# Kernel tuning notes

Measured on AMD Instinct MI355X. Metric: run time of the kernel, lower is better.

Reference implementation:

```python
import jax, jax.numpy as jnp
import numpy as np

B, S, HID, NH = 4, 1024, 1024, 16
HD = HID // NH  # 64


def setup_inputs() -> dict:
    key = jax.random.key(0)
    ks = jax.random.split(key, 8)
    scale = 0.02
    return {
        "attention_mask": jnp.zeros((B, 1, 1, S), dtype=jnp.float32),
        "query": jax.random.normal(ks[0], (B, S, HID), dtype=jnp.float32),
        "key": jax.random.normal(ks[1], (B, S, HID), dtype=jnp.float32),
        "value": jax.random.normal(ks[2], (B, S, HID), dtype=jnp.float32),
        "Wq": jax.random.normal(ks[3], (HID, HID), dtype=jnp.float32) * scale,
        "bq": jnp.zeros((HID,), dtype=jnp.float32),
        "Wk": jax.random.normal(ks[4], (HID, HID), dtype=jnp.float32) * scale,
        "bk": jnp.zeros((HID,), dtype=jnp.float32),
    }


def reference(attention_mask, query, key, value, Wq, bq, Wk, bk):
    # Linear projections (torch Linear: x @ W.T + b)
    q = query @ Wq.T + bq  # [B,S,HID]
    k = key @ Wk.T + bk    # [B,S,HID]
    # split heads -> [B,NH,S,HD]
    q = q.reshape(B, S, NH, HD).transpose(0, 2, 1, 3)
    k = k.reshape(B, S, NH, HD).transpose(0, 2, 1, 3)
    scores = jnp.einsum("bhqd,bhkd->bhqk", q, k) / jnp.sqrt(jnp.float32(HD))
    scores = scores + attention_mask  # additive mask broadcast [B,1,1,S]
    probs = jax.nn.softmax(scores, axis=-1)  # [B,NH,S,S]
    # V is shared across heads; head-mean folds into a single contraction:
    # mean_h(probs_h @ V) = (sum_h probs_h) @ V / NH
    out = jnp.einsum("bhqk,bkv->bqv", probs, value) / NH  # [B,S,HID]
    return out
```

## Files before the change

kernel.cpp:

```cpp
#include <hip/hip_runtime.h>
#include <hip/hip_fp16.h>

#define B_    4
#define S_    1024
#define HID_  1024
#define NH_   16
#define HD_   64

#define LOG2E 1.44269504f
#define PSTR  40

typedef _Float16 half8 __attribute__((ext_vector_type(8)));
typedef float f32x4 __attribute__((ext_vector_type(4)));

__device__ __forceinline__ half8 cvt8(float4 a, float4 b) {
    half8 h;
    h[0] = (_Float16)a.x; h[1] = (_Float16)a.y;
    h[2] = (_Float16)a.z; h[3] = (_Float16)a.w;
    h[4] = (_Float16)b.x; h[5] = (_Float16)b.y;
    h[6] = (_Float16)b.z; h[7] = (_Float16)b.w;
    return h;
}

__device__ __forceinline__ float fexp2(float x) {
#if __has_builtin(__builtin_amdgcn_exp2f)
    return __builtin_amdgcn_exp2f(x);
#else
    float r;
    asm("v_exp_f32 %0, %1\n\ts_nop 0" : "=v"(r) : "v"(x));
    return r;
#endif
}

__device__ __forceinline__ void lds_barrier() {
    asm volatile("s_waitcnt lgkmcnt(0)" ::: "memory");
    __builtin_amdgcn_s_barrier();
    __builtin_amdgcn_sched_barrier(0);
}

__device__ __forceinline__ void gll16(const _Float16* g, _Float16* l) {
    __builtin_amdgcn_global_load_lds(
        (const __attribute__((address_space(1))) unsigned int*)g,
        (__attribute__((address_space(3))) unsigned int*)l, 16, 0, 0);
}

__global__ __launch_bounds__(256) void cast_f16(
    const float* __restrict__ query, const float* __restrict__ key,
    const float* __restrict__ Wq, const float* __restrict__ Wk,
    _Float16* __restrict__ Af16, _Float16* __restrict__ Wf16)
{
    const int x = blockIdx.x;
    if (blockIdx.y == 0) {
        long base = ((long)x * 256 + threadIdx.x) * 8;
        const float* src = (x < 2048) ? (query + base) : (key + base - (4l << 20));
        float4 v0 = *(const float4*)src, v1 = *(const float4*)(src + 4);
        *(half8*)(Af16 + base) = cvt8(v0, v1);
    } else {
        if (x >= 1024) return;
        long base = ((long)x * 256 + threadIdx.x) * 8;
        const float* src = (x < 512) ? (Wq + base) : (Wk + base - (1l << 20));
        float4 v0 = *(const float4*)src, v1 = *(const float4*)(src + 4);
        *(half8*)(Wf16 + base) = cvt8(v0, v1);
    }
}

__global__ __launch_bounds__(256) void proj_qk_f16(
    const _Float16* __restrict__ Af16,
    const _Float16* __restrict__ Wf16,
    const float* __restrict__ bq, const float* __restrict__ bk,
    _Float16* __restrict__ Oq, _Float16* __restrict__ Ok)
{
    const int f  = blockIdx.x + 16 * blockIdx.y + 512 * blockIdx.z;
    const int w2 = (f & 7) * 128 + (f >> 3);
    const int bx = w2 & 15, by = (w2 >> 4) & 31, bz = w2 >> 9;

    const _Float16* A    = Af16 + (long)bz * 4096 * 1024;
    const _Float16* Wm   = Wf16 + (long)bz * 1024 * 1024;
    const float*    bias = bz ? bk : bq;
    _Float16*       Co   = bz ? Ok : Oq;

    __shared__ _Float16 Al[2][128 * 32];
    __shared__ _Float16 Bl[2][64 * 32];

    const int tid  = threadIdx.x;
    const int wv   = tid >> 6;
    const int lane = tid & 63;
    const int l15  = lane & 15;
    const int quad = lane >> 4;
    const int wm   = wv & 1, wn = wv >> 1;
    const int m0   = by * 128, n0 = bx * 64;

    const int srA  = (lane >> 2);
    const int scA  = (lane & 3) * 8;
    const _Float16* gA0 = A  + (long)(m0 + wv * 16 + srA) * 1024 + scA;
    const _Float16* gA1 = A  + (long)(m0 + 64 + wv * 16 + srA) * 1024 + scA;
    const _Float16* gB  = Wm + (long)(n0 + wv * 16 + srA) * 1024 + scA;
    const int ldsW = wv * 512;

    f32x4 acc[4][2];
#pragma unroll
    for (int i = 0; i < 4; i++)
#pragma unroll
        for (int j = 0; j < 2; j++) acc[i][j] = (f32x4){0.f, 0.f, 0.f, 0.f};

    gll16(gA0, &Al[0][ldsW]);
    gll16(gA1, &Al[0][2048 + ldsW]);
    gll16(gB,  &Bl[0][ldsW]);
    __syncthreads();

#pragma unroll 2
    for (int kt = 0; kt < HID_; kt += 32) {
        const int p = (kt >> 5) & 1;

        if (kt + 32 < HID_) {
            gll16(gA0 + kt + 32, &Al[p ^ 1][ldsW]);
            gll16(gA1 + kt + 32, &Al[p ^ 1][2048 + ldsW]);
            gll16(gB  + kt + 32, &Bl[p ^ 1][ldsW]);
        }

        half8 af[4], bf[2];
#pragma unroll
        for (int i = 0; i < 4; i++)
            af[i] = *(const half8*)(&Al[p][(wm * 64 + i * 16 + l15) * 32 + quad * 8]);
#pragma unroll
        for (int j = 0; j < 2; j++)
            bf[j] = *(const half8*)(&Bl[p][(wn * 32 + j * 16 + l15) * 32 + quad * 8]);

#pragma unroll
        for (int i = 0; i < 4; i++)
#pragma unroll
            for (int j = 0; j < 2; j++)
                acc[i][j] = __builtin_amdgcn_mfma_f32_16x16x32_f16(
                    af[i], bf[j], acc[i][j], 0, 0, 0);

        __syncthreads();
    }

    const int isQ = (bz == 0);
#pragma unroll
    for (int j = 0; j < 2; j++) {
        int col = n0 + wn * 32 + j * 16 + l15;
        float bv = bias[col];
        int h = col >> 6, d = col & 63, pp = d >> 3, jj = d & 7;
#pragma unroll
        for (int i = 0; i < 4; i++) {
            int row = m0 + wm * 64 + i * 16 + quad * 4;
            int bb = row >> 10, ss = row & 1023;
            long base;
            if (isQ)
                base = ((((long)(bb * NH_ + h) * 64 + (ss >> 4)) * 8 + pp) * 16
                        + (ss & 15)) * 8 + jj;
            else
                base = (((long)(bb * NH_ + h) * 8 + pp) * 1024 + ss) * 8 + jj;
#pragma unroll
            for (int r = 0; r < 4; r++)
                Co[base + r * 8] = (_Float16)(acc[i][j][r] + bv);
        }
    }
}

__global__ __launch_bounds__(512) void attn_psum_f16(
    const _Float16* __restrict__ qb,
    const _Float16* __restrict__ kb,
    const float* __restrict__ mask,
    _Float16* __restrict__ P)
{
    const int f   = blockIdx.x + 64 * blockIdx.y + 256 * blockIdx.z;
    const int w2s = (f & 7) * 128 + (f >> 3);
    const int qt  = w2s & 63;
    const int b   = (w2s >> 6) & 3;
    const int hz  = w2s >> 8;

    const int q0   = qt * 16;
    const int tid  = threadIdx.x;
    const int w    = tid >> 6;
    const int lane = tid & 63;
    const int l15  = lane & 15;
    const int quad = lane >> 4;

    __shared__ float redS[2][16][8];

    const float SC = 0.125f * LOG2E;

    float mreg[8];
#pragma unroll
    for (int t = 0; t < 8; t++)
        mreg[t] = mask[b * S_ + t * 128 + w * 16 + l15] * LOG2E;

    f32x4 acc[8];
#pragma unroll
    for (int t = 0; t < 8; t++) acc[t] = (f32x4){0.f, 0.f, 0.f, 0.f};

    for (int ii = 0; ii < 4; ii++) {
        const int h = hz * 4 + ii;
        const _Float16* qh = qb + ((long)(b * NH_ + h) * 64 + qt) * 1024;
        const _Float16* kh = kb + (long)(b * NH_ + h) * 8192 * 8;

        half8 a0 = *(const half8*)(qh + quad * 128 + l15 * 8);
        half8 a1 = *(const half8*)(qh + (quad + 4) * 128 + l15 * 8);

        f32x4 s[8];
#pragma unroll
        for (int cc = 0; cc < 8; cc++) {
            const int key = cc * 128 + w * 16 + l15;
            half8 b0 = *(const half8*)(kh + (long)quad * 8192 + key * 8);
            half8 b1 = *(const half8*)(kh + (long)(quad + 4) * 8192 + key * 8);
            f32x4 c = (f32x4){0.f, 0.f, 0.f, 0.f};
            c = __builtin_amdgcn_mfma_f32_16x16x32_f16(a0, b0, c, 0, 0, 0);
            c = __builtin_amdgcn_mfma_f32_16x16x32_f16(a1, b1, c, 0, 0, 0);
            s[cc] = c;
        }

        const int p = ii & 1;
        float sm[4] = {0.f, 0.f, 0.f, 0.f};
#pragma unroll
        for (int t = 0; t < 8; t++)
#pragma unroll
            for (int r = 0; r < 4; r++) {
                float pr = fexp2(fmaf(s[t][r], SC, mreg[t]));
                s[t][r] = pr;
                sm[r] += pr;
            }
#pragma unroll
        for (int off = 1; off < 16; off <<= 1)
#pragma unroll
            for (int r = 0; r < 4; r++) sm[r] += __shfl_xor(sm[r], off);
        if (l15 == 0)
#pragma unroll
            for (int r = 0; r < 4; r++) redS[p][quad * 4 + r][w] = sm[r];
        __syncthreads();

#pragma unroll
        for (int r = 0; r < 4; r++) {
            float4 v0 = *(float4*)&redS[p][quad * 4 + r][0];
            float4 v1 = *(float4*)&redS[p][quad * 4 + r][4];
            float tot = (v0.x + v0.y + v0.z + v0.w) + (v1.x + v1.y + v1.z + v1.w);
            float inv = 1.f / tot;
#pragma unroll
            for (int t = 0; t < 8; t++) acc[t][r] += s[t][r] * inv;
        }
    }

    _Float16* prow = P + (long)hz * ((long)B_ * S_ * S_) + (long)(b * S_ + q0) * S_;
#pragma unroll
    for (int t = 0; t < 8; t++)
#pragma unroll
        for (int r = 0; r < 4; r++) {
            int row = quad * 4 + r;
            prow[(long)row * S_ + t * 128 + w * 16 + l15] = (_Float16)acc[t][r];
        }
}

__global__ __launch_bounds__(256) void vt_combine(
    const _Float16* __restrict__ P, _Float16* __restrict__ o,
    const float* __restrict__ V, _Float16* __restrict__ Vt)
{
    __shared__ float t[32][33];
    if (blockIdx.y == 0) {
        if (blockIdx.x >= 2048) return;
        const long QS = (long)B_ * S_ * S_;
        long i = (long)(blockIdx.x * 256 + threadIdx.x) * 8;
        half8 a = *(const half8*)(P + i);
        half8 b = *(const half8*)(P + QS + i);
        half8 c = *(const half8*)(P + 2 * QS + i);
        half8 d = *(const half8*)(P + 3 * QS + i);
        half8 r;
#pragma unroll
        for (int e = 0; e < 8; e++)
            r[e] = (_Float16)((float)a[e] + (float)b[e] + (float)c[e] + (float)d[e]);
        *(half8*)(o + i) = r;
    } else {
        const int x  = blockIdx.x;
        const int b  = x >> 10;
        const int s0 = ((x >> 5) & 31) * 32;
        const int h0 = (x & 31) * 32;
        const int tx = threadIdx.x & 31, ty = threadIdx.x >> 5;
#pragma unroll
        for (int rr = 0; rr < 4; rr++) {
            int s = s0 + ty + rr * 8;
            t[ty + rr * 8][tx] = V[((long)b * S_ + s) * HID_ + h0 + tx];
        }
        __syncthreads();
#pragma unroll
        for (int rr = 0; rr < 4; rr++) {
            int h = h0 + ty + rr * 8;
            Vt[((long)b * HID_ + h) * S_ + s0 + tx] = (_Float16)t[tx][ty + rr * 8];
        }
    }
}

__global__ __launch_bounds__(256) void pv_f16(
    const _Float16* __restrict__ Pc,
    const _Float16* __restrict__ Vt,
    float* __restrict__ out)
{
    const int f   = blockIdx.x + 16 * blockIdx.y + 128 * blockIdx.z;
    const int xcd = f & 7, ii = f >> 3;
    const int bx  = ii & 15;
    const int by  = (ii >> 4) + ((xcd & 1) << 2);
    const int b   = xcd >> 1;

    const _Float16* A  = Pc + (long)b * S_ * S_;
    const _Float16* Bm = Vt + (long)b * HID_ * S_;

    __shared__ _Float16 Al[2][128 * PSTR];
    __shared__ _Float16 Bl[2][64 * PSTR];

    const int tid  = threadIdx.x;
    const int wv   = tid >> 6;
    const int lane = tid & 63;
    const int l15  = lane & 15;
    const int quad = lane >> 4;
    const int wm   = wv & 1, wn = wv >> 1;
    const int m0   = by * 128, n0 = bx * 64;
    const int sr   = tid >> 2;
    const int sc   = (tid & 3) * 8;

    const _Float16* ap0 = A  + (long)(m0 + sr) * S_ + sc;
    const _Float16* ap1 = A  + (long)(m0 + 64 + sr) * S_ + sc;
    const _Float16* bp0 = Bm + (long)(n0 + sr) * S_ + sc;

    f32x4 acc[4][2];
#pragma unroll
    for (int i = 0; i < 4; i++)
#pragma unroll
        for (int j = 0; j < 2; j++) acc[i][j] = (f32x4){0.f, 0.f, 0.f, 0.f};

    half8 ca0 = *(const half8*)(ap0);
    half8 ca1 = *(const half8*)(ap1);
    half8 cb0 = *(const half8*)(bp0);
    *(half8*)&Al[0][sr * PSTR + sc] = ca0;
    *(half8*)&Al[0][(64 + sr) * PSTR + sc] = ca1;
    *(half8*)&Bl[0][sr * PSTR + sc] = cb0;
    ca0 = *(const half8*)(ap0 + 32);
    ca1 = *(const half8*)(ap1 + 32);
    cb0 = *(const half8*)(bp0 + 32);
    lds_barrier();

#pragma unroll 2
    for (int kt = 0; kt < S_; kt += 32) {
        const int p = (kt >> 5) & 1;

        half8 na0 = ca0, na1 = ca1, nb0 = cb0;
        if (kt + 64 < S_) {
            na0 = *(const half8*)(ap0 + kt + 64);
            na1 = *(const half8*)(ap1 + kt + 64);
            nb0 = *(const half8*)(bp0 + kt + 64);
        }

        half8 af[4], bfm[2];
#pragma unroll
        for (int i = 0; i < 4; i++)
            af[i] = *(const half8*)(&Al[p][(wm * 64 + i * 16 + l15) * PSTR + quad * 8]);
#pragma unroll
        for (int j = 0; j < 2; j++)
            bfm[j] = *(const half8*)(&Bl[p][(wn * 32 + j * 16 + l15) * PSTR + quad * 8]);

        if (kt + 32 < S_) {
            *(half8*)&Al[p ^ 1][sr * PSTR + sc] = ca0;
            *(half8*)&Al[p ^ 1][(64 + sr) * PSTR + sc] = ca1;
            *(half8*)&Bl[p ^ 1][sr * PSTR + sc] = cb0;
        }

#pragma unroll
        for (int i = 0; i < 4; i++)
#pragma unroll
            for (int j = 0; j < 2; j++)
                acc[i][j] = __builtin_amdgcn_mfma_f32_16x16x32_f16(
                    af[i], bfm[j], acc[i][j], 0, 0, 0);

        lds_barrier();
        ca0 = na0; ca1 = na1; cb0 = nb0;
    }

    const float alpha = 1.f / NH_;
#pragma unroll
    for (int i = 0; i < 4; i++) {
        int row = m0 + wm * 64 + i * 16 + quad * 4;
#pragma unroll
        for (int j = 0; j < 2; j++) {
            int col = n0 + wn * 32 + j * 16 + l15;
#pragma unroll
            for (int r = 0; r < 4; r++)
                out[(long)(b * S_ + row + r) * HID_ + col] = acc[i][j][r] * alpha;
        }
    }
}

extern "C" void kernel_launch(void* const* d_in, const int* in_sizes, int n_in,
                              void* d_out, int out_size, void* d_ws, size_t ws_size,
                              hipStream_t stream)
{
    const float* mask  = (const float*)d_in[0];
    const float* query = (const float*)d_in[1];
    const float* key   = (const float*)d_in[2];
    const float* value = (const float*)d_in[3];
    const float* Wq    = (const float*)d_in[4];
    const float* bq    = (const float*)d_in[5];
    const float* Wk    = (const float*)d_in[6];
    const float* bk    = (const float*)d_in[7];
    float* out = (float*)d_out;

    char* ws = (char*)d_ws;
    const long MB = 1l << 20;
    _Float16* qbuf = (_Float16*)(ws);
    _Float16* kbuf = (_Float16*)(ws + 8 * MB);
    _Float16* Af16 = (_Float16*)(ws + 16 * MB);
    _Float16* Wf16 = (_Float16*)(ws + 32 * MB);
    _Float16* Pq   = (_Float16*)(ws + 16 * MB);
    _Float16* Vt   = (_Float16*)(ws);
    _Float16* psum = (_Float16*)(ws + 8 * MB);

    cast_f16<<<dim3(4096, 2), dim3(256), 0, stream>>>(
        query, key, Wq, Wk, Af16, Wf16);

    proj_qk_f16<<<dim3(16, 32, 2), dim3(256), 0, stream>>>(
        Af16, Wf16, bq, bk, qbuf, kbuf);

    attn_psum_f16<<<dim3(S_ / 16, B_, 4), dim3(512), 0, stream>>>(
        qbuf, kbuf, mask, Pq);

    vt_combine<<<dim3(4096, 2), dim3(256), 0, stream>>>(Pq, psum, value, Vt);

    pv_f16<<<dim3(HID_ / 64, S_ / 128, B_), dim3(256), 0, stream>>>(psum, Vt, out);
}
```

Before: 196.3 us.

## Sum all heads in one attention pass, move V transpose into cast, use direct-to-LDS loads

The attention kernel now loops over all 16 heads per block and writes the head-summed probabilities directly. This removes the four partial P buffers and the separate combine pass, along with their large memory traffic. The V transpose moves into the cast kernel, and the PV GEMM switches to global_load_lds direct-to-LDS loads with an unpadded layout. The cost is a much smaller attention grid (256 blocks of 512 threads), which may underfill the GPU and serialize 16 heads per block. The unpadded LDS layout may also cause bank conflicts.

```diff
diff --git a/kernel.cpp b/kernel.cpp
--- a/kernel.cpp
+++ b/kernel.cpp
@@ -8,7 +8,6 @@
 #define HD_   64
 
 #define LOG2E 1.44269504f
-#define PSTR  40
 
 typedef _Float16 half8 __attribute__((ext_vector_type(8)));
 typedef float f32x4 __attribute__((ext_vector_type(4)));
@@ -32,12 +31,6 @@
 #endif
 }
 
-__device__ __forceinline__ void lds_barrier() {
-    asm volatile("s_waitcnt lgkmcnt(0)" ::: "memory");
-    __builtin_amdgcn_s_barrier();
-    __builtin_amdgcn_sched_barrier(0);
-}
-
 __device__ __forceinline__ void gll16(const _Float16* g, _Float16* l) {
     __builtin_amdgcn_global_load_lds(
         (const __attribute__((address_space(1))) unsigned int*)g,
@@ -47,20 +40,39 @@
 __global__ __launch_bounds__(256) void cast_f16(
     const float* __restrict__ query, const float* __restrict__ key,
     const float* __restrict__ Wq, const float* __restrict__ Wk,
-    _Float16* __restrict__ Af16, _Float16* __restrict__ Wf16)
-{
+    const float* __restrict__ V,
+    _Float16* __restrict__ Af16, _Float16* __restrict__ Wf16,
+    _Float16* __restrict__ Vt)
+{
+    __shared__ float t[32][33];
     const int x = blockIdx.x;
     if (blockIdx.y == 0) {
         long base = ((long)x * 256 + threadIdx.x) * 8;
         const float* src = (x < 2048) ? (query + base) : (key + base - (4l << 20));
         float4 v0 = *(const float4*)src, v1 = *(const float4*)(src + 4);
         *(half8*)(Af16 + base) = cvt8(v0, v1);
-    } else {
+    } else if (blockIdx.y == 1) {
         if (x >= 1024) return;
         long base = ((long)x * 256 + threadIdx.x) * 8;
         const float* src = (x < 512) ? (Wq + base) : (Wk + base - (1l << 20));
         float4 v0 = *(const float4*)src, v1 = *(const float4*)(src + 4);
         *(half8*)(Wf16 + base) = cvt8(v0, v1);
+    } else {
+        const int b  = x >> 10;
+        const int s0 = ((x >> 5) & 31) * 32;
+        const int h0 = (x & 31) * 32;
+        const int tx = threadIdx.x & 31, ty = threadIdx.x >> 5;
+#pragma unroll
+        for (int rr = 0; rr < 4; rr++) {
+            int s = s0 + ty + rr * 8;
+            t[ty + rr * 8][tx] = V[((long)b * S_ + s) * HID_ + h0 + tx];
+        }
+        __syncthreads();
+#pragma unroll
+        for (int rr = 0; rr < 4; rr++) {
+            int h = h0 + ty + rr * 8;
+            Vt[((long)b * HID_ + h) * S_ + s0 + tx] = (_Float16)t[tx][ty + rr * 8];
+        }
     }
 }
 
@@ -163,13 +175,12 @@
     const _Float16* __restrict__ qb,
     const _Float16* __restrict__ kb,
     const float* __restrict__ mask,
-    _Float16* __restrict__ P)
-{
-    const int f   = blockIdx.x + 64 * blockIdx.y + 256 * blockIdx.z;
-    const int w2s = (f & 7) * 128 + (f >> 3);
+    _Float16* __restrict__ psum)
+{
+    const int f   = blockIdx.x + 64 * blockIdx.y;
+    const int w2s = (f & 7) * 32 + (f >> 3);
     const int qt  = w2s & 63;
-    const int b   = (w2s >> 6) & 3;
-    const int hz  = w2s >> 8;
+    const int b   = w2s >> 6;
 
     const int q0   = qt * 16;
     const int tid  = threadIdx.x;
@@ -191,8 +202,7 @@
 #pragma unroll
     for (int t = 0; t < 8; t++) acc[t] = (f32x4){0.f, 0.f, 0.f, 0.f};
 
-    for (int ii = 0; ii < 4; ii++) {
-        const int h = hz * 4 + ii;
+    for (int h = 0; h < NH_; h++) {
         const _Float16* qh = qb + ((long)(b * NH_ + h) * 64 + qt) * 1024;
         const _Float16* kh = kb + (long)(b * NH_ + h) * 8192 * 8;
 
@@ -211,7 +221,7 @@
             s[cc] = c;
         }
 
-        const int p = ii & 1;
+        const int p = h & 1;
         float sm[4] = {0.f, 0.f, 0.f, 0.f};
 #pragma unroll
         for (int t = 0; t < 8; t++)
@@ -241,7 +251,7 @@
         }
     }
 
-    _Float16* prow = P + (long)hz * ((long)B_ * S_ * S_) + (long)(b * S_ + q0) * S_;
+    _Float16* prow = psum + (long)(b * S_ + q0) * S_;
 #pragma unroll
     for (int t = 0; t < 8; t++)
 #pragma unroll
@@ -249,44 +259,6 @@
             int row = quad * 4 + r;
             prow[(long)row * S_ + t * 128 + w * 16 + l15] = (_Float16)acc[t][r];
         }
-}
-
-__global__ __launch_bounds__(256) void vt_combine(
-    const _Float16* __restrict__ P, _Float16* __restrict__ o,
-    const float* __restrict__ V, _Float16* __restrict__ Vt)
-{
-    __shared__ float t[32][33];
-    if (blockIdx.y == 0) {
-        if (blockIdx.x >= 2048) return;
-        const long QS = (long)B_ * S_ * S_;
-        long i = (long)(blockIdx.x * 256 + threadIdx.x) * 8;
-        half8 a = *(const half8*)(P + i);
-        half8 b = *(const half8*)(P + QS + i);
-        half8 c = *(const half8*)(P + 2 * QS + i);
-        half8 d = *(const half8*)(P + 3 * QS + i);
-        half8 r;
-#pragma unroll
-        for (int e = 0; e < 8; e++)
-            r[e] = (_Float16)((float)a[e] + (float)b[e] + (float)c[e] + (float)d[e]);
-        *(half8*)(o + i) = r;
-    } else {
-        const int x  = blockIdx.x;
-        const int b  = x >> 10;
-        const int s0 = ((x >> 5) & 31) * 32;
-        const int h0 = (x & 31) * 32;
-        const int tx = threadIdx.x & 31, ty = threadIdx.x >> 5;
-#pragma unroll
-        for (int rr = 0; rr < 4; rr++) {
-            int s = s0 + ty + rr * 8;
-            t[ty + rr * 8][tx] = V[((long)b * S_ + s) * HID_ + h0 + tx];
-        }
-        __syncthreads();
-#pragma unroll
-        for (int rr = 0; rr < 4; rr++) {
-            int h = h0 + ty + rr * 8;
-            Vt[((long)b * HID_ + h) * S_ + s0 + tx] = (_Float16)t[tx][ty + rr * 8];
-        }
-    }
 }
 
 __global__ __launch_bounds__(256) void pv_f16(
@@ -303,8 +275,8 @@
     const _Float16* A  = Pc + (long)b * S_ * S_;
     const _Float16* Bm = Vt + (long)b * HID_ * S_;
 
-    __shared__ _Float16 Al[2][128 * PSTR];
-    __shared__ _Float16 Bl[2][64 * PSTR];
+    __shared__ _Float16 Al[2][128 * 32];
+    __shared__ _Float16 Bl[2][64 * 32];
 
     const int tid  = threadIdx.x;
     const int wv   = tid >> 6;
@@ -313,12 +285,13 @@
     const int quad = lane >> 4;
     const int wm   = wv & 1, wn = wv >> 1;
     const int m0   = by * 128, n0 = bx * 64;
-    const int sr   = tid >> 2;
-    const int sc   = (tid & 3) * 8;
-
-    const _Float16* ap0 = A  + (long)(m0 + sr) * S_ + sc;
-    const _Float16* ap1 = A  + (long)(m0 + 64 + sr) * S_ + sc;
-    const _Float16* bp0 = Bm + (long)(n0 + sr) * S_ + sc;
+
+    const int srA  = (lane >> 2);
+    const int scA  = (lane & 3) * 8;
+    const _Float16* gA0 = A  + (long)(m0 + wv * 16 + srA) * S_ + scA;
+    const _Float16* gA1 = A  + (long)(m0 + 64 + wv * 16 + srA) * S_ + scA;
+    const _Float16* gB  = Bm + (long)(n0 + wv * 16 + srA) * S_ + scA;
+    const int ldsW = wv * 512;
 
     f32x4 acc[4][2];
 #pragma unroll
@@ -326,51 +299,37 @@
 #pragma unroll
         for (int j = 0; j < 2; j++) acc[i][j] = (f32x4){0.f, 0.f, 0.f, 0.f};
 
-    half8 ca0 = *(const half8*)(ap0);
-    half8 ca1 = *(const half8*)(ap1);
-    half8 cb0 = *(const half8*)(bp0);
-    *(half8*)&Al[0][sr * PSTR + sc] = ca0;
-    *(half8*)&Al[0][(64 + sr) * PSTR + sc] = ca1;
-    *(half8*)&Bl[0][sr * PSTR + sc] = cb0;
-    ca0 = *(const half8*)(ap0 + 32);
-    ca1 = *(const half8*)(ap1 + 32);
-    cb0 = *(const half8*)(bp0 + 32);
-    lds_barrier();
+    gll16(gA0, &Al[0][ldsW]);
+    gll16(gA1, &Al[0][2048 + ldsW]);
+    gll16(gB,  &Bl[0][ldsW]);
+    __syncthreads();
 
 #pragma unroll 2
     for (int kt = 0; kt < S_; kt += 32) {
         const int p = (kt >> 5) & 1;
 
-        half8 na0 = ca0, na1 = ca1, nb0 = cb0;
-        if (kt + 64 < S_) {
-            na0 = *(const half8*)(ap0 + kt + 64);
-            na1 = *(const half8*)(ap1 + kt + 64);
-            nb0 = *(const half8*)(bp0 + kt + 64);
-        }
-
-        half8 af[4], bfm[2];
+        if (kt + 32 < S_) {
+            gll16(gA0 + kt + 32, &Al[p ^ 1][ldsW]);
+            gll16(gA1 + kt + 32, &Al[p ^ 1][2048 + ldsW]);
+            gll16(gB  + kt + 32, &Bl[p ^ 1][ldsW]);
+        }
+
+        half8 af[4], bf[2];
 #pragma unroll
         for (int i = 0; i < 4; i++)
-            af[i] = *(const half8*)(&Al[p][(wm * 64 + i * 16 + l15) * PSTR + quad * 8]);
+            af[i] = *(const half8*)(&Al[p][(wm * 64 + i * 16 + l15) * 32 + quad * 8]);
 #pragma unroll
         for (int j = 0; j < 2; j++)
-            bfm[j] = *(const half8*)(&Bl[p][(wn * 32 + j * 16 + l15) * PSTR + quad * 8]);
-
-        if (kt + 32 < S_) {
-            *(half8*)&Al[p ^ 1][sr * PSTR + sc] = ca0;
-            *(half8*)&Al[p ^ 1][(64 + sr) * PSTR + sc] = ca1;
-            *(half8*)&Bl[p ^ 1][sr * PSTR + sc] = cb0;
-        }
+            bf[j] = *(const half8*)(&Bl[p][(wn * 32 + j * 16 + l15) * 32 + quad * 8]);
 
 #pragma unroll
         for (int i = 0; i < 4; i++)
 #pragma unroll
             for (int j = 0; j < 2; j++)
                 acc[i][j] = __builtin_amdgcn_mfma_f32_16x16x32_f16(
-                    af[i], bfm[j], acc[i][j], 0, 0, 0);
-
-        lds_barrier();
-        ca0 = na0; ca1 = na1; cb0 = nb0;
+                    af[i], bf[j], acc[i][j], 0, 0, 0);
+
+        __syncthreads();
     }
 
     const float alpha = 1.f / NH_;
@@ -407,20 +366,17 @@
     _Float16* kbuf = (_Float16*)(ws + 8 * MB);
     _Float16* Af16 = (_Float16*)(ws + 16 * MB);
     _Float16* Wf16 = (_Float16*)(ws + 32 * MB);
-    _Float16* Pq   = (_Float16*)(ws + 16 * MB);
-    _Float16* Vt   = (_Float16*)(ws);
-    _Float16* psum = (_Float16*)(ws + 8 * MB);
-
-    cast_f16<<<dim3(4096, 2), dim3(256), 0, stream>>>(
-        query, key, Wq, Wk, Af16, Wf16);
+    _Float16* Vt   = (_Float16*)(ws + 36 * MB);
+    _Float16* psum = (_Float16*)(ws + 16 * MB);
+
+    cast_f16<<<dim3(4096, 3), dim3(256), 0, stream>>>(
+        query, key, Wq, Wk, value, Af16, Wf16, Vt);
 
     proj_qk_f16<<<dim3(16, 32, 2), dim3(256), 0, stream>>>(
         Af16, Wf16, bq, bk, qbuf, kbuf);
 
-    attn_psum_f16<<<dim3(S_ / 16, B_, 4), dim3(512), 0, stream>>>(
-        qbuf, kbuf, mask, Pq);
-
-    vt_combine<<<dim3(4096, 2), dim3(256), 0, stream>>>(Pq, psum, value, Vt);
-
-    pv_f16<<<dim3(HID_ / 64, S_ / 128, B_), dim3(256), 0, stream>>>(psum, Vt, out);
-}
+    attn_psum_f16<<<dim3(64, B_), dim3(512), 0, stream>>>(
+        qbuf, kbuf, mask, psum);
+
+    pv_f16<<<dim3(16, 8, B_), dim3(256), 0, stream>>>(psum, Vt, out);
+}
```

Result: slower. 202.6 us (+3.2%).
